# Optimization experiments

Hardware: AMD Instinct MI355X
Metric: run time of the kernel (lower is better)

Reference implementation:

```python
import jax, jax.numpy as jnp
import numpy as np

N = 100_000          # num nodes
E = 1_600_000        # undirected edges (mean_degree = 2E/N = 32)
Q = 8                # num_groups
NUM_ITER = 5         # fixed BP iterations (max_num_iter)


def setup_inputs() -> dict:
    key = jax.random.key(0)
    k1, k2, k3, k4 = jax.random.split(key, 4)
    u = jax.random.randint(k1, (E,), 0, N, dtype=jnp.int32)
    v = jax.random.randint(k2, (E,), 0, N, dtype=jnp.int32)
    # directed messages: both orientations of every undirected edge
    src = jnp.concatenate([u, v])                 # [2E] message source i of i->j
    dst = jnp.concatenate([v, u])                 # [2E] message target j of i->j
    # rev[e] = index of the reverse message j->i for edge e = i->j
    rev = jnp.concatenate([jnp.arange(E, 2 * E, dtype=jnp.int32),
                           jnp.arange(E, dtype=jnp.int32)])
    psi0 = jax.random.uniform(k3, (N, Q), dtype=jnp.float32)
    msg0 = jax.random.uniform(k4, (2 * E, Q), dtype=jnp.float32)
    c = 2.0 * E / N  # mean degree
    beta = jnp.asarray(np.log(Q / np.sqrt(c - 1.0) + 1.0), dtype=jnp.float32)
    return dict(beta=beta, psi0=psi0, msg0=msg0, src=src, dst=dst, rev=rev,
                num_iter=NUM_ITER)


def reference(beta, psi0, msg0, src, dst, rev, num_iter):
    N_, Q_ = psi0.shape
    M = msg0.shape[0]
    mean_w = M / (N_ * N_)  # adjacency_matrix.mean() = 2E / N^2 (unweighted)
    psi = psi0 / psi0.sum(1, keepdims=True)   # normalized marginals [N,Q]
    msg = msg0 / msg0.sum(1, keepdims=True)   # normalized messages  [M,Q]
    h = (-beta * mean_w * psi).sum(0)         # external field        [Q]

    def step(carry, _):
        msg, psi, h = carry
        c = jnp.expm1(beta)                          # e^beta - 1
        # per-incoming-edge factor, in log space (scatter_mul -> segment_sum of logs)
        log_f = jnp.log1p(msg * c)                   # [M,Q]
        S = jax.ops.segment_sum(log_f, dst, num_segments=N_)  # [N,Q] prod over k->i
        # message i->j: exclude contribution of reverse edge j->i (cavity)
        logits = h + S[src] - log_f[rev]             # [M,Q]
        new_msg = jax.nn.softmax(logits, axis=-1)    # normalized per message
        diff = jnp.max(jnp.abs(new_msg - msg))
        # marginals from updated messages
        log_f2 = jnp.log1p(new_msg * c)
        S2 = jax.ops.segment_sum(log_f2, dst, num_segments=N_)
        new_psi = jax.nn.softmax(h + S2, axis=-1)    # [N,Q]
        new_h = (-beta * mean_w * new_psi).sum(0)    # [Q]
        return (new_msg, new_psi, new_h), diff

    (msg, psi, h), diffs = jax.lax.scan(step, (msg, psi, h), None, length=int(num_iter))
    return msg, psi, diffs[-1]
```

## Files before the change

### kernel.cpp

```cpp
#include <hip/hip_runtime.h>
#include <math.h>

#define Q 8
#define NUM_ITER 5
#define BLOCK 256
#define EBLK 1024
#define BLOCKA 512
#define NBN 1024
#define NBSHIFT 10
#define MAXBKT 128
#define W 4
#define QS 262144.0f
#define GRED 512

__device__ __forceinline__ void load8(const float* __restrict__ p, float v[Q]) {
    float4 a = ((const float4*)p)[0];
    float4 b = ((const float4*)p)[1];
    v[0]=a.x; v[1]=a.y; v[2]=a.z; v[3]=a.w;
    v[4]=b.x; v[5]=b.y; v[6]=b.z; v[7]=b.w;
}

__device__ __forceinline__ void store8(float* __restrict__ p, const float v[Q]) {
    ((float4*)p)[0] = make_float4(v[0],v[1],v[2],v[3]);
    ((float4*)p)[1] = make_float4(v[4],v[5],v[6],v[7]);
}

__device__ __forceinline__ void softmax8_fast(float l[Q]) {
    float mx = l[0];
    #pragma unroll
    for (int q=1;q<Q;q++) mx = fmaxf(mx, l[q]);
    float s = 0.f;
    #pragma unroll
    for (int q=0;q<Q;q++) { l[q] = __expf(l[q]-mx); s += l[q]; }
    float inv = 1.0f/s;
    #pragma unroll
    for (int q=0;q<Q;q++) l[q] *= inv;
}

__device__ __forceinline__ void pack18(const float lf[Q], int loc, uint4& a, unsigned& x) {
    unsigned v[Q];
    #pragma unroll
    for (int q=0;q<Q;q++) v[q] = (unsigned)__float2int_rn(lf[q]*QS);
    a.x = (v[0]&0xFFFFu) | ((v[1]&0xFFFFu)<<16);
    a.y = (v[2]&0xFFFFu) | ((v[3]&0xFFFFu)<<16);
    a.z = (v[4]&0xFFFFu) | ((v[5]&0xFFFFu)<<16);
    a.w = (v[6]&0xFFFFu) | ((v[7]&0xFFFFu)<<16);
    x = (v[0]>>16) | ((v[1]>>16)<<2) | ((v[2]>>16)<<4) | ((v[3]>>16)<<6)
      | ((v[4]>>16)<<8) | ((v[5]>>16)<<10) | ((v[6]>>16)<<12) | ((v[7]>>16)<<14)
      | ((unsigned)loc<<16);
}

__device__ __forceinline__ void dq18(uint4 a, unsigned x, float lf[Q]) {
    lf[0] = (float)((a.x & 0xFFFFu) | ((x     &3u)<<16)) * (1.0f/QS);
    lf[1] = (float)((a.x >> 16)     | (((x>>2 )&3u)<<16)) * (1.0f/QS);
    lf[2] = (float)((a.y & 0xFFFFu) | (((x>>4 )&3u)<<16)) * (1.0f/QS);
    lf[3] = (float)((a.y >> 16)     | (((x>>6 )&3u)<<16)) * (1.0f/QS);
    lf[4] = (float)((a.z & 0xFFFFu) | (((x>>8 )&3u)<<16)) * (1.0f/QS);
    lf[5] = (float)((a.z >> 16)     | (((x>>10)&3u)<<16)) * (1.0f/QS);
    lf[6] = (float)((a.w & 0xFFFFu) | (((x>>12)&3u)<<16)) * (1.0f/QS);
    lf[7] = (float)((a.w >> 16)     | (((x>>14)&3u)<<16)) * (1.0f/QS);
}

__global__ void k_count(const int* __restrict__ src, const int* __restrict__ dst,
                        int* __restrict__ bcnt, int E, int nbkt) {
    __shared__ int c[4][MAXBKT];
    int wv = threadIdx.x >> 6;
    for (int t=threadIdx.x; t<4*MAXBKT; t+=BLOCK) ((int*)c)[t]=0;
    __syncthreads();
    for (int k = blockIdx.x*BLOCK + threadIdx.x; k < E; k += gridDim.x*BLOCK) {
        atomicAdd(&c[wv][dst[k]>>NBSHIFT], 1);
        atomicAdd(&c[wv][src[k]>>NBSHIFT], 1);
    }
    __syncthreads();
    for (int t=threadIdx.x; t<nbkt; t+=BLOCK) {
        int s = c[0][t]+c[1][t]+c[2][t]+c[3][t];
        if (s) atomicAdd(&bcnt[t], s);
    }
}

__global__ void k_scan(const int* __restrict__ bcnt, int* __restrict__ bucket_start,
                       int* __restrict__ cursor_g, int nbkt) {
    if (threadIdx.x==0 && blockIdx.x==0) {
        int run = 0;
        for (int b=0;b<nbkt;b++) { bucket_start[b]=run; cursor_g[b*16]=run; run += bcnt[b]; }
        bucket_start[nbkt] = run;
    }
}

__global__ void k_psi_init(const float* __restrict__ psi0,
                           const float* __restrict__ beta_p,
                           float mean_w, double* __restrict__ h0, int N) {
    int i = blockIdx.x*BLOCK + threadIdx.x;
    float c[Q];
    #pragma unroll
    for (int q=0;q<Q;q++) c[q]=0.f;
    if (i < N) {
        float p[Q]; load8(psi0 + (size_t)i*Q, p);
        float s = 0.f;
        #pragma unroll
        for (int q=0;q<Q;q++) s += p[q];
        float scale = -beta_p[0]*mean_w/s;
        #pragma unroll
        for (int q=0;q<Q;q++) c[q] = p[q]*scale;
    }
    __shared__ double sm[BLOCK/64][Q];
    #pragma unroll
    for (int q=0;q<Q;q++) {
        double x = (double)c[q];
        #pragma unroll
        for (int off=32;off;off>>=1) x += __shfl_down(x,off);
        if ((threadIdx.x&63)==0) sm[threadIdx.x>>6][q]=x;
    }
    __syncthreads();
    if (threadIdx.x < Q) {
        double x = sm[0][threadIdx.x]+sm[1][threadIdx.x]+sm[2][threadIdx.x]+sm[3][threadIdx.x];
        atomicAdd(h0+threadIdx.x, x);
    }
}

__global__ __launch_bounds__(EBLK) void k_init(const float* __restrict__ msg0,
                       const int* __restrict__ src, const int* __restrict__ dst,
                       const float* __restrict__ beta_p,
                       uint4* __restrict__ lfe_q, unsigned* __restrict__ lfe_x,
                       uint4* __restrict__ ebuf_q, unsigned* __restrict__ ebuf_x,
                       int* __restrict__ cursor_g, int E, int nbkt) {
    __shared__ int cnt[MAXBKT], excl[MAXBKT], base[MAXBKT];
    __shared__ int totsh;
    __shared__ uint4 staged[2*EBLK];
    __shared__ unsigned staged_x[2*EBLK];
    __shared__ int gpos[2*EBLK];
    int tid = threadIdx.x;
    for (int t=tid; t<MAXBKT; t+=EBLK) cnt[t]=0;
    __syncthreads();
    int k = blockIdx.x*EBLK + tid;
    bool act = (k < E);
    int b1=0,b2=0,o1=0,o2=0;
    uint4 p1, p2; unsigned x1, x2;
    if (act) {
        float cc = expm1f(beta_p[0]);
        int i = src[k], j = dst[k];
        float a[Q], b[Q];
        load8(msg0 + (size_t)k*Q, a);
        load8(msg0 + ((size_t)k+E)*Q, b);
        float sa=0.f, sb=0.f;
        #pragma unroll
        for (int q=0;q<Q;q++) { sa += a[q]; sb += b[q]; }
        float ia = 1.0f/sa, ib = 1.0f/sb;
        #pragma unroll
        for (int q=0;q<Q;q++) { a[q]*=ia; b[q]*=ib; }
        float lfa[Q], lfb[Q];
        #pragma unroll
        for (int q=0;q<Q;q++) {
            lfa[q] = __logf(fmaf(a[q], cc, 1.0f));
            lfb[q] = __logf(fmaf(b[q], cc, 1.0f));
        }
        b1 = j>>NBSHIFT; b2 = i>>NBSHIFT;
        o1 = atomicAdd(&cnt[b1], 1);
        o2 = atomicAdd(&cnt[b2], 1);
        pack18(lfa, j & (NBN-1), p1, x1);
        pack18(lfb, i & (NBN-1), p2, x2);
        lfe_q[k]   = p1; lfe_x[k]   = x1;
        lfe_q[k+E] = p2; lfe_x[k+E] = x2;
    }
    __syncthreads();
    if (tid < 64) {
        int a = cnt[2*tid], b = cnt[2*tid+1];
        int s = a+b;
        int incl = s;
        #pragma unroll
        for (int d=1; d<64; d<<=1) {
            int v = __shfl_up(incl, d);
            if (tid >= d) incl += v;
        }
        int exclp = incl - s;
        excl[2*tid]   = exclp;
        excl[2*tid+1] = exclp + a;
        if (tid==63) totsh = incl;
        base[2*tid]   = a ? atomicAdd(&cursor_g[(2*tid)*16], a) : 0;
        base[2*tid+1] = b ? atomicAdd(&cursor_g[(2*tid+1)*16], b) : 0;
    }
    __syncthreads();
    if (act) {
        int s1 = excl[b1]+o1; staged[s1]=p1; staged_x[s1]=x1; gpos[s1]=base[b1]+o1;
        int s2 = excl[b2]+o2; staged[s2]=p2; staged_x[s2]=x2; gpos[s2]=base[b2]+o2;
    }
    __syncthreads();
    int total = totsh;
    for (int s=tid; s<total; s+=EBLK) {
        int g = gpos[s];
        ebuf_q[g] = staged[s];
        ebuf_x[g] = staged_x[s];
    }
}

template<bool LAST>
__global__ __launch_bounds__(EBLK) void k_edge(const int* __restrict__ src,
                       const int* __restrict__ dst,
                       const float* __restrict__ beta_p,
                       const double* __restrict__ h, const float* __restrict__ Sf,
                       uint4* __restrict__ lfe_q, unsigned* __restrict__ lfe_x,
                       float* __restrict__ out_msg,
                       uint4* __restrict__ ebuf_q, unsigned* __restrict__ ebuf_x,
                       int* __restrict__ cursor_g,
                       float* __restrict__ diff_out,
                       int E, int nbkt) {
    __shared__ int cnt[MAXBKT], excl[MAXBKT], base[MAXBKT];
    __shared__ int totsh;
    __shared__ uint4 staged[2*EBLK];
    __shared__ unsigned staged_x[2*EBLK];
    __shared__ int gpos[2*EBLK];
    int tid = threadIdx.x;
    for (int t=tid; t<MAXBKT; t+=EBLK) cnt[t]=0;
    __syncthreads();
    int k = blockIdx.x*EBLK + tid;
    bool act = (k < E);
    float lmax = 0.f;
    int b1=0,b2=0,o1=0,o2=0;
    uint4 p1, p2; unsigned x1, x2;
    if (act) {
        float cc = expm1f(beta_p[0]);
        int i = src[k], j = dst[k];
        float lf1o[Q], lf2o[Q];
        dq18(lfe_q[k],   lfe_x[k],   lf1o);
        dq18(lfe_q[k+E], lfe_x[k+E], lf2o);
        float hv[Q];
        #pragma unroll
        for (int q=0;q<Q;q++) hv[q] = (float)h[q];
        float Si[Q], Sj[Q];
        load8(Sf + (size_t)i*Q, Si);
        load8(Sf + (size_t)j*Q, Sj);
        float l1[Q], l2[Q];
        #pragma unroll
        for (int q=0;q<Q;q++) {
            l1[q] = hv[q] + Si[q] - lf2o[q];
            l2[q] = hv[q] + Sj[q] - lf1o[q];
        }
        softmax8_fast(l1);
        softmax8_fast(l2);
        if (LAST) {
            float icc = 1.0f/cc;
            #pragma unroll
            for (int q=0;q<Q;q++) {
                float m1o = (__expf(lf1o[q]) - 1.0f) * icc;
                float m2o = (__expf(lf2o[q]) - 1.0f) * icc;
                lmax = fmaxf(lmax, fabsf(l1[q]-m1o));
                lmax = fmaxf(lmax, fabsf(l2[q]-m2o));
            }
            store8(out_msg + (size_t)k*Q,     l1);
            store8(out_msg + ((size_t)k+E)*Q, l2);
        }
        float lf1n[Q], lf2n[Q];
        #pragma unroll
        for (int q=0;q<Q;q++) {
            lf1n[q] = __logf(fmaf(l1[q], cc, 1.0f));
            lf2n[q] = __logf(fmaf(l2[q], cc, 1.0f));
        }
        b1 = j>>NBSHIFT; b2 = i>>NBSHIFT;
        o1 = atomicAdd(&cnt[b1], 1);
        o2 = atomicAdd(&cnt[b2], 1);
        pack18(lf1n, j & (NBN-1), p1, x1);
        pack18(lf2n, i & (NBN-1), p2, x2);
        lfe_q[k]   = p1; lfe_x[k]   = x1;
        lfe_q[k+E] = p2; lfe_x[k+E] = x2;
    }
    __syncthreads();
    if (tid < 64) {
        int a = cnt[2*tid], b = cnt[2*tid+1];
        int s = a+b;
        int incl = s;
        #pragma unroll
        for (int d=1; d<64; d<<=1) {
            int v = __shfl_up(incl, d);
            if (tid >= d) incl += v;
        }
        int exclp = incl - s;
        excl[2*tid]   = exclp;
        excl[2*tid+1] = exclp + a;
        if (tid==63) totsh = incl;
        base[2*tid]   = a ? atomicAdd(&cursor_g[(2*tid)*16], a) : 0;
        base[2*tid+1] = b ? atomicAdd(&cursor_g[(2*tid+1)*16], b) : 0;
    }
    __syncthreads();
    if (act) {
        int s1 = excl[b1]+o1; staged[s1]=p1; staged_x[s1]=x1; gpos[s1]=base[b1]+o1;
        int s2 = excl[b2]+o2; staged[s2]=p2; staged_x[s2]=x2; gpos[s2]=base[b2]+o2;
    }
    __syncthreads();
    int total = totsh;
    for (int s=tid; s<total; s+=EBLK) {
        int g = gpos[s];
        ebuf_q[g] = staged[s];
        ebuf_x[g] = staged_x[s];
    }
    if (LAST) {
        float x = lmax;
        #pragma unroll
        for (int off=32;off;off>>=1) x = fmaxf(x, __shfl_down(x,off));
        __shared__ float smx[EBLK/64];
        if ((tid&63)==0) smx[tid>>6]=x;
        __syncthreads();
        if (tid==0) {
            float bmax = smx[0];
            #pragma unroll
            for (int t=1;t<EBLK/64;t++) bmax = fmaxf(bmax, smx[t]);
            atomicMax((unsigned int*)diff_out, __float_as_uint(bmax));
        }
    }
}

__global__ __launch_bounds__(BLOCKA) void k_accum(const uint4* __restrict__ ebuf_q,
                                                  const unsigned* __restrict__ ebuf_x,
                                                  const int* __restrict__ bucket_start,
                                                  unsigned long long* __restrict__ partials,
                                                  int* __restrict__ cursor_g) {
    __shared__ unsigned long long Sl[NBN*4];
    int wg = blockIdx.x;
    int b = wg / W, w = wg % W;
    for (int t=threadIdx.x*4; t<NBN*8; t+=BLOCKA*4) *(int4*)((int*)Sl+t) = make_int4(0,0,0,0);
    int lo = bucket_start[b], hi = bucket_start[b+1];
    if (w==0 && threadIdx.x==0) cursor_g[b*16] = lo;
    __syncthreads();
    int len = hi - lo;
    int l0 = lo + (int)(((long long)len * w) / W);
    int l1 = lo + (int)(((long long)len * (w+1)) / W);
    for (int s = l0 + threadIdx.x; s < l1; s += BLOCKA) {
        uint4 v = ebuf_q[s];
        unsigned x = ebuf_x[s];
        int loc = (int)(x >> 16);
        unsigned long long v0 = (v.x&0xFFFFu) | ((x&3u)<<16);
        unsigned long long v1 = (v.x>>16)     | (((x>>2)&3u)<<16);
        unsigned long long v2 = (v.y&0xFFFFu) | (((x>>4)&3u)<<16);
        unsigned long long v3 = (v.y>>16)     | (((x>>6)&3u)<<16);
        unsigned long long v4 = (v.z&0xFFFFu) | (((x>>8)&3u)<<16);
        unsigned long long v5 = (v.z>>16)     | (((x>>10)&3u)<<16);
        unsigned long long v6 = (v.w&0xFFFFu) | (((x>>12)&3u)<<16);
        unsigned long long v7 = (v.w>>16)     | (((x>>14)&3u)<<16);
        unsigned long long* p = Sl + loc*4;
        atomicAdd(p+0, v0 | (v1<<32));
        atomicAdd(p+1, v2 | (v3<<32));
        atomicAdd(p+2, v4 | (v5<<32));
        atomicAdd(p+3, v6 | (v7<<32));
    }
    __syncthreads();
    unsigned long long* outp = partials + (size_t)wg * (NBN*4);
    for (int t=threadIdx.x*4; t<NBN*8; t+=BLOCKA*4) *(int4*)((int*)outp+t) = *(const int4*)((const int*)Sl+t);
}

template<bool INIT, bool LAST>
__global__ __launch_bounds__(BLOCK) void k_reduce(const unsigned* __restrict__ pu,
                         const double* __restrict__ hcur,
                         const float* __restrict__ beta_p,
                         float mean_w, double* __restrict__ hnext,
                         float* __restrict__ Sf, float* __restrict__ psi_out, int N) {
    int q = threadIdx.x & 7;
    float hq = 0.f;
    if (!INIT) hq = (float)hcur[q];
    double pacc = 0.0;
    int total = N*8;
    int stride = BLOCK*GRED;
    for (int gid = blockIdx.x*BLOCK + threadIdx.x; gid < total; gid += stride) {
        int i = gid >> 3;
        int b = i >> NBSHIFT, loc = i & (NBN-1);
        unsigned s = 0;
        #pragma unroll
        for (int w=0; w<W; ++w) s += pu[(size_t)(b*W+w)*(NBN*8) + loc*8 + q];
        float Sv = (float)s * (1.0f/QS);
        Sf[gid] = Sv;
        if (!INIT) {
            float l = hq + Sv;
            float mx = l;
            #pragma unroll
            for (int m8=1;m8<8;m8<<=1) mx = fmaxf(mx, __shfl_xor(mx, m8));
            float ex = __expf(l - mx);
            float sum = ex;
            #pragma unroll
            for (int m8=1;m8<8;m8<<=1) sum += __shfl_xor(sum, m8);
            float p = ex / sum;
            if (LAST) psi_out[gid] = p;
            pacc += (double)p;
        }
    }
    if (!INIT) {
        double x = pacc;
        #pragma unroll
        for (int m8=8;m8<64;m8<<=1) x += __shfl_xor(x, m8);
        __shared__ double sm[BLOCK/64][Q];
        if ((threadIdx.x&63) < Q) sm[threadIdx.x>>6][threadIdx.x&7] = x;
        __syncthreads();
        if (threadIdx.x < Q) {
            double t = sm[0][threadIdx.x]+sm[1][threadIdx.x]+sm[2][threadIdx.x]+sm[3][threadIdx.x];
            double scale = -(double)beta_p[0]*(double)mean_w;
            atomicAdd(hnext+threadIdx.x, t*scale);
        }
    }
}

extern "C" void kernel_launch(void* const* d_in, const int* in_sizes, int n_in,
                              void* d_out, int out_size, void* d_ws, size_t ws_size,
                              hipStream_t stream) {
    const float* beta = (const float*)d_in[0];
    const float* psi0 = (const float*)d_in[1];
    const float* msg0 = (const float*)d_in[2];
    const int*   src  = (const int*)d_in[3];
    const int*   dst  = (const int*)d_in[4];

    int N = in_sizes[1] / Q;
    int M = in_sizes[2] / Q;
    int E = M / 2;
    int nbkt = (N + NBN - 1) / NBN;
    float mean_w = (float)((double)M / ((double)N * (double)N));

    float* out_msg  = (float*)d_out;
    float* out_psi  = out_msg + (size_t)M*Q;
    float* out_diff = out_psi + (size_t)N*Q;

    char* p = (char*)d_ws;
    double* hb[2];
    hb[0] = (double*)p;                      p += 2*Q*sizeof(double);
    hb[1] = hb[0] + Q;
    unsigned long long* partials = (unsigned long long*)p;  p += (size_t)nbkt*W*NBN*4*sizeof(unsigned long long);
    float* Sf = (float*)p;                   p += (size_t)N*Q*sizeof(float);
    uint4* lfe_q = (uint4*)p;                p += (size_t)M*sizeof(uint4);
    uint4* ebuf_q = (uint4*)p;               p += (size_t)M*sizeof(uint4);
    unsigned* lfe_x = (unsigned*)p;          p += (size_t)M*sizeof(unsigned);
    unsigned* ebuf_x = (unsigned*)p;         p += (size_t)M*sizeof(unsigned);
    int* bcnt = (int*)p;                     p += MAXBKT*sizeof(int);
    int* bucket_start = (int*)p;             p += (MAXBKT+1)*sizeof(int);
    int* cursor_g = (int*)p;

    int geE   = (E + EBLK-1)/EBLK;
    int gn    = (N + BLOCK-1)/BLOCK;
    int gacc  = nbkt * W;

    hipMemsetAsync(hb[0], 0, Q*sizeof(double), stream);
    hipMemsetAsync(bcnt, 0, MAXBKT*sizeof(int), stream);

    k_count<<<256,BLOCK,0,stream>>>(src, dst, bcnt, E, nbkt);
    k_scan<<<1,64,0,stream>>>(bcnt, bucket_start, cursor_g, nbkt);
    k_init<<<geE,EBLK,0,stream>>>(msg0, src, dst, beta, lfe_q, lfe_x, ebuf_q, ebuf_x,
                                  cursor_g, E, nbkt);
    k_psi_init<<<gn,BLOCK,0,stream>>>(psi0, beta, mean_w, hb[0], N);
    k_accum<<<gacc,BLOCKA,0,stream>>>(ebuf_q, ebuf_x, bucket_start, partials, cursor_g);
    k_reduce<true,false><<<GRED,BLOCK,0,stream>>>((const unsigned*)partials, hb[0], beta,
                                                  mean_w, hb[1], Sf, out_psi, N);

    int cur = 0;
    for (int t=0; t<NUM_ITER; ++t) {
        int nxt = cur^1;
        hipMemsetAsync(hb[nxt], 0, Q*sizeof(double), stream);
        if (t == NUM_ITER-1) {
            hipMemsetAsync(out_diff, 0, sizeof(float), stream);
            k_edge<true ><<<geE,EBLK,0,stream>>>(src,dst,beta,hb[cur],Sf,lfe_q,lfe_x,out_msg,
                                                 ebuf_q,ebuf_x,cursor_g,out_diff,E,nbkt);
            k_accum<<<gacc,BLOCKA,0,stream>>>(ebuf_q, ebuf_x, bucket_start, partials, cursor_g);
            k_reduce<false,true ><<<GRED,BLOCK,0,stream>>>((const unsigned*)partials, hb[cur], beta,
                                                           mean_w, hb[nxt], Sf, out_psi, N);
        } else {
            k_edge<false><<<geE,EBLK,0,stream>>>(src,dst,beta,hb[cur],Sf,lfe_q,lfe_x,out_msg,
                                                 ebuf_q,ebuf_x,cursor_g,out_diff,E,nbkt);
            k_accum<<<gacc,BLOCKA,0,stream>>>(ebuf_q, ebuf_x, bucket_start, partials, cursor_g);
            k_reduce<false,false><<<GRED,BLOCK,0,stream>>>((const unsigned*)partials, hb[cur], beta,
                                                           mean_w, hb[nxt], Sf, out_psi, N);
        }
        cur = nxt;
    }
}
```

Baseline: 619.8 us.

## Replace atomic bucket cursors with precomputed per-block scatter offsets

Computes per-block, per-bucket counts once up front and scans them, so every edge-kernel block reads a fixed base offset instead of claiming one with global atomics on shared cursors. This removes the per-block atomic contention and the cursor reset in the accumulate kernel, and makes the bucket layout deterministic. It costs extra setup kernels and workspace for the count and offset tables, and relies on the edge ordering per block being the same every iteration, which holds here because it depends only on src/dst.

```diff
diff --git a/kernel.cpp b/kernel.cpp
--- a/kernel.cpp
+++ b/kernel.cpp
@@ -61,28 +61,54 @@
     lf[7] = (float)((a.w >> 16)     | (((x>>14)&3u)<<16)) * (1.0f/QS);
 }
 
-__global__ void k_count(const int* __restrict__ src, const int* __restrict__ dst,
-                        int* __restrict__ bcnt, int E, int nbkt) {
-    __shared__ int c[4][MAXBKT];
-    int wv = threadIdx.x >> 6;
-    for (int t=threadIdx.x; t<4*MAXBKT; t+=BLOCK) ((int*)c)[t]=0;
-    __syncthreads();
-    for (int k = blockIdx.x*BLOCK + threadIdx.x; k < E; k += gridDim.x*BLOCK) {
-        atomicAdd(&c[wv][dst[k]>>NBSHIFT], 1);
-        atomicAdd(&c[wv][src[k]>>NBSHIFT], 1);
-    }
-    __syncthreads();
-    for (int t=threadIdx.x; t<nbkt; t+=BLOCK) {
-        int s = c[0][t]+c[1][t]+c[2][t]+c[3][t];
-        if (s) atomicAdd(&bcnt[t], s);
-    }
-}
-
-__global__ void k_scan(const int* __restrict__ bcnt, int* __restrict__ bucket_start,
-                       int* __restrict__ cursor_g, int nbkt) {
+__global__ __launch_bounds__(EBLK) void k_cnt2(const int* __restrict__ src,
+                                               const int* __restrict__ dst,
+                                               int* __restrict__ gcnt, int E) {
+    __shared__ int cnt[MAXBKT];
+    int tid = threadIdx.x;
+    for (int t=tid; t<MAXBKT; t+=EBLK) cnt[t]=0;
+    __syncthreads();
+    int k = blockIdx.x*EBLK + tid;
+    if (k < E) {
+        atomicAdd(&cnt[dst[k]>>NBSHIFT], 1);
+        atomicAdd(&cnt[src[k]>>NBSHIFT], 1);
+    }
+    __syncthreads();
+    for (int t=tid; t<MAXBKT; t+=EBLK) gcnt[(size_t)blockIdx.x*MAXBKT + t] = cnt[t];
+}
+
+__global__ __launch_bounds__(256) void k_scan2(const int* __restrict__ gcnt,
+                                               int* __restrict__ erel,
+                                               int* __restrict__ btot, int nblk) {
+    int b = blockIdx.x;
+    int t = threadIdx.x;
+    int chunk = (nblk + 255) / 256;
+    int lo = t*chunk, hi = lo+chunk; if (hi > nblk) hi = nblk; if (lo > nblk) lo = nblk;
+    int s = 0;
+    for (int i=lo;i<hi;++i) s += gcnt[(size_t)i*MAXBKT + b];
+    __shared__ int part[256];
+    part[t] = s;
+    __syncthreads();
+    for (int off=1; off<256; off<<=1) {
+        int v = (t>=off) ? part[t-off] : 0;
+        __syncthreads();
+        part[t] += v;
+        __syncthreads();
+    }
+    int base = (t==0) ? 0 : part[t-1];
+    for (int i=lo;i<hi;++i) {
+        int c = gcnt[(size_t)i*MAXBKT + b];
+        erel[(size_t)i*MAXBKT + b] = base;
+        base += c;
+    }
+    if (t==255) btot[b] = part[255];
+}
+
+__global__ void k_scan(const int* __restrict__ btot, int* __restrict__ bucket_start,
+                       int nbkt) {
     if (threadIdx.x==0 && blockIdx.x==0) {
         int run = 0;
-        for (int b=0;b<nbkt;b++) { bucket_start[b]=run; cursor_g[b*16]=run; run += bcnt[b]; }
+        for (int b=0;b<nbkt;b++) { bucket_start[b]=run; run += btot[b]; }
         bucket_start[nbkt] = run;
     }
 }
@@ -123,7 +149,8 @@
                        const float* __restrict__ beta_p,
                        uint4* __restrict__ lfe_q, unsigned* __restrict__ lfe_x,
                        uint4* __restrict__ ebuf_q, unsigned* __restrict__ ebuf_x,
-                       int* __restrict__ cursor_g, int E, int nbkt) {
+                       const int* __restrict__ erel,
+                       const int* __restrict__ bucket_start_g, int E) {
     __shared__ int cnt[MAXBKT], excl[MAXBKT], base[MAXBKT];
     __shared__ int totsh;
     __shared__ uint4 staged[2*EBLK];
@@ -131,6 +158,7 @@
     __shared__ int gpos[2*EBLK];
     int tid = threadIdx.x;
     for (int t=tid; t<MAXBKT; t+=EBLK) cnt[t]=0;
+    if (tid < MAXBKT) base[tid] = bucket_start_g[tid] + erel[(size_t)blockIdx.x*MAXBKT + tid];
     __syncthreads();
     int k = blockIdx.x*EBLK + tid;
     bool act = (k < E);
@@ -176,8 +204,6 @@
         excl[2*tid]   = exclp;
         excl[2*tid+1] = exclp + a;
         if (tid==63) totsh = incl;
-        base[2*tid]   = a ? atomicAdd(&cursor_g[(2*tid)*16], a) : 0;
-        base[2*tid+1] = b ? atomicAdd(&cursor_g[(2*tid+1)*16], b) : 0;
     }
     __syncthreads();
     if (act) {
@@ -201,9 +227,9 @@
                        uint4* __restrict__ lfe_q, unsigned* __restrict__ lfe_x,
                        float* __restrict__ out_msg,
                        uint4* __restrict__ ebuf_q, unsigned* __restrict__ ebuf_x,
-                       int* __restrict__ cursor_g,
-                       float* __restrict__ diff_out,
-                       int E, int nbkt) {
+                       const int* __restrict__ erel,
+                       const int* __restrict__ bucket_start_g,
+                       float* __restrict__ diff_out, int E) {
     __shared__ int cnt[MAXBKT], excl[MAXBKT], base[MAXBKT];
     __shared__ int totsh;
     __shared__ uint4 staged[2*EBLK];
@@ -211,6 +237,7 @@
     __shared__ int gpos[2*EBLK];
     int tid = threadIdx.x;
     for (int t=tid; t<MAXBKT; t+=EBLK) cnt[t]=0;
+    if (tid < MAXBKT) base[tid] = bucket_start_g[tid] + erel[(size_t)blockIdx.x*MAXBKT + tid];
     __syncthreads();
     int k = blockIdx.x*EBLK + tid;
     bool act = (k < E);
@@ -277,8 +304,6 @@
         excl[2*tid]   = exclp;
         excl[2*tid+1] = exclp + a;
         if (tid==63) totsh = incl;
-        base[2*tid]   = a ? atomicAdd(&cursor_g[(2*tid)*16], a) : 0;
-        base[2*tid+1] = b ? atomicAdd(&cursor_g[(2*tid+1)*16], b) : 0;
     }
     __syncthreads();
     if (act) {
@@ -311,15 +336,13 @@
 __global__ __launch_bounds__(BLOCKA) void k_accum(const uint4* __restrict__ ebuf_q,
                                                   const unsigned* __restrict__ ebuf_x,
                                                   const int* __restrict__ bucket_start,
-                                                  unsigned long long* __restrict__ partials,
-                                                  int* __restrict__ cursor_g) {
+                                                  unsigned long long* __restrict__ partials) {
     __shared__ unsigned long long Sl[NBN*4];
     int wg = blockIdx.x;
     int b = wg / W, w = wg % W;
     for (int t=threadIdx.x*4; t<NBN*8; t+=BLOCKA*4) *(int4*)((int*)Sl+t) = make_int4(0,0,0,0);
+    __syncthreads();
     int lo = bucket_start[b], hi = bucket_start[b+1];
-    if (w==0 && threadIdx.x==0) cursor_g[b*16] = lo;
-    __syncthreads();
     int len = hi - lo;
     int l0 = lo + (int)(((long long)len * w) / W);
     int l1 = lo + (int)(((long long)len * (w+1)) / W);
@@ -414,6 +437,8 @@
     float* out_psi  = out_msg + (size_t)M*Q;
     float* out_diff = out_psi + (size_t)N*Q;
 
+    int geE = (E + EBLK-1)/EBLK;
+
     char* p = (char*)d_ws;
     double* hb[2];
     hb[0] = (double*)p;                      p += 2*Q*sizeof(double);
@@ -424,23 +449,24 @@
     uint4* ebuf_q = (uint4*)p;               p += (size_t)M*sizeof(uint4);
     unsigned* lfe_x = (unsigned*)p;          p += (size_t)M*sizeof(unsigned);
     unsigned* ebuf_x = (unsigned*)p;         p += (size_t)M*sizeof(unsigned);
-    int* bcnt = (int*)p;                     p += MAXBKT*sizeof(int);
+    int* gcnt = (int*)p;                     p += (size_t)geE*MAXBKT*sizeof(int);
+    int* erel = (int*)p;                     p += (size_t)geE*MAXBKT*sizeof(int);
+    int* btot = (int*)p;                     p += MAXBKT*sizeof(int);
     int* bucket_start = (int*)p;             p += (MAXBKT+1)*sizeof(int);
-    int* cursor_g = (int*)p;
-
-    int geE   = (E + EBLK-1)/EBLK;
-    int gn    = (N + BLOCK-1)/BLOCK;
-    int gacc  = nbkt * W;
+
+    int gn   = (N + BLOCK-1)/BLOCK;
+    int gacc = nbkt * W;
 
     hipMemsetAsync(hb[0], 0, Q*sizeof(double), stream);
-    hipMemsetAsync(bcnt, 0, MAXBKT*sizeof(int), stream);
-
-    k_count<<<256,BLOCK,0,stream>>>(src, dst, bcnt, E, nbkt);
-    k_scan<<<1,64,0,stream>>>(bcnt, bucket_start, cursor_g, nbkt);
+
+    k_cnt2<<<geE,EBLK,0,stream>>>(src, dst, gcnt, E);
+    k_scan2<<<nbkt,256,0,stream>>>(gcnt, erel, btot, geE);
+    k_scan<<<1,64,0,stream>>>(btot, bucket_start, nbkt);
+
     k_init<<<geE,EBLK,0,stream>>>(msg0, src, dst, beta, lfe_q, lfe_x, ebuf_q, ebuf_x,
-                                  cursor_g, E, nbkt);
+                                  erel, bucket_start, E);
     k_psi_init<<<gn,BLOCK,0,stream>>>(psi0, beta, mean_w, hb[0], N);
-    k_accum<<<gacc,BLOCKA,0,stream>>>(ebuf_q, ebuf_x, bucket_start, partials, cursor_g);
+    k_accum<<<gacc,BLOCKA,0,stream>>>(ebuf_q, ebuf_x, bucket_start, partials);
     k_reduce<true,false><<<GRED,BLOCK,0,stream>>>((const unsigned*)partials, hb[0], beta,
                                                   mean_w, hb[1], Sf, out_psi, N);
 
@@ -451,14 +477,14 @@
         if (t == NUM_ITER-1) {
             hipMemsetAsync(out_diff, 0, sizeof(float), stream);
             k_edge<true ><<<geE,EBLK,0,stream>>>(src,dst,beta,hb[cur],Sf,lfe_q,lfe_x,out_msg,
-                                                 ebuf_q,ebuf_x,cursor_g,out_diff,E,nbkt);
-            k_accum<<<gacc,BLOCKA,0,stream>>>(ebuf_q, ebuf_x, bucket_start, partials, cursor_g);
+                                                 ebuf_q,ebuf_x,erel,bucket_start,out_diff,E);
+            k_accum<<<gacc,BLOCKA,0,stream>>>(ebuf_q, ebuf_x, bucket_start, partials);
             k_reduce<false,true ><<<GRED,BLOCK,0,stream>>>((const unsigned*)partials, hb[cur], beta,
                                                            mean_w, hb[nxt], Sf, out_psi, N);
         } else {
             k_edge<false><<<geE,EBLK,0,stream>>>(src,dst,beta,hb[cur],Sf,lfe_q,lfe_x,out_msg,
-                                                 ebuf_q,ebuf_x,cursor_g,out_diff,E,nbkt);
-            k_accum<<<gacc,BLOCKA,0,stream>>>(ebuf_q, ebuf_x, bucket_start, partials, cursor_g);
+                                                 ebuf_q,ebuf_x,erel,bucket_start,out_diff,E);
+            k_accum<<<gacc,BLOCKA,0,stream>>>(ebuf_q, ebuf_x, bucket_start, partials);
             k_reduce<false,false><<<GRED,BLOCK,0,stream>>>((const unsigned*)partials, hb[cur], beta,
                                                            mean_w, hb[nxt], Sf, out_psi, N);
         }
```

After: 579.3 us. -6.5%, faster.
